# Optimization experiments

Hardware: AMD Instinct MI355X
Metric: run time of the kernel (lower is better)

Reference implementation:

```python
import jax, jax.numpy as jnp
import numpy as np

BATCH, BITS, HID = 65536, 64, 512
EPS = 1e-5

# M[s, i, j] = 1 if j == i - s  (left-shift-by-s permutation, causal)
_SHIFT_M = jnp.asarray(
    (np.arange(BITS)[None, :, None] - np.arange(BITS)[:, None, None]
     == np.arange(BITS)[None, None, :]).astype(np.float32))


def _layernorm(x, g, b):
    m = jnp.mean(x, axis=-1, keepdims=True)
    v = jnp.var(x, axis=-1, keepdims=True)
    return (x - m) * jax.lax.rsqrt(v + EPS) * g + b


def setup_inputs() -> dict:
    key = jax.random.key(0)
    ks = jax.random.split(key, 8)
    inp = {
        'a_bits': jax.random.uniform(ks[0], (BATCH, BITS), dtype=jnp.float32),
        'shift_bits': jax.random.uniform(ks[1], (BATCH, BITS), dtype=jnp.float32),
        # shift_decoder params: Linear(64,512) -> LN -> GELU -> Linear(512,512) -> LN -> GELU -> Linear(512,64)
        'W1': jax.random.normal(ks[2], (BITS, HID), dtype=jnp.float32) * (1.0 / np.sqrt(BITS)),
        'b1': jnp.zeros((HID,), jnp.float32),
        'g1': jnp.ones((HID,), jnp.float32),
        'be1': jnp.zeros((HID,), jnp.float32),
        'W2': jax.random.normal(ks[3], (HID, HID), dtype=jnp.float32) * (1.0 / np.sqrt(HID)),
        'b2': jnp.zeros((HID,), jnp.float32),
        'g2': jnp.ones((HID,), jnp.float32),
        'be2': jnp.zeros((HID,), jnp.float32),
        'W3': jax.random.normal(ks[4], (HID, BITS), dtype=jnp.float32) * (1.0 / np.sqrt(HID)),
        'b3': jnp.zeros((BITS,), jnp.float32),
    }
    return inp


def reference(a_bits, shift_bits, W1, b1, g1, be1, W2, b2, g2, be2, W3, b3):
    temperature = jnp.float32(1.0)
    # shift decoder MLP
    h = jax.nn.gelu(_layernorm(shift_bits @ W1 + b1, g1, be1), approximate=False)
    h = jax.nn.gelu(_layernorm(h @ W2 + b2, g2, be2), approximate=False)
    shift_logits = (h @ W3 + b3)[:, :BITS]
    # training path: soft shift distribution
    shift_probs = jax.nn.softmax(shift_logits / temperature, axis=-1)
    # weighted permutation matrix, then batched matvec (faithful to einsum+bmm)
    M_weighted = jnp.einsum('bs,sij->bij', shift_probs, _SHIFT_M)
    output = jnp.einsum('bij,bj->bi', M_weighted, a_bits)
    return output
```

## Files before the change

kernel.cpp:

```cpp
#include <hip/hip_runtime.h>
#include <hip/hip_bf16.h>
#include <math.h>

#define BATCH 65536
#define NT 512
#define BM 32

using f32x4 = __attribute__((ext_vector_type(4))) float;
using s16x8 = __attribute__((ext_vector_type(8))) short;

#define MFMA16(a, b, c) __builtin_amdgcn_mfma_f32_16x16x32_bf16((a), (b), (c), 0, 0, 0)

__device__ __forceinline__ unsigned short f2bf(float f) {
    unsigned u = __builtin_bit_cast(unsigned, f);
    u = u + 0x7FFFu + ((u >> 16) & 1u);
    return (unsigned short)(u >> 16);
}
__device__ __forceinline__ float bf2f(unsigned short h) {
    unsigned u = ((unsigned)h) << 16;
    return __builtin_bit_cast(float, u);
}

__device__ __forceinline__ float fast_erf(float x) {
    float ax = fabsf(x);
    float t = __builtin_amdgcn_rcpf(fmaf(0.3275911f, ax, 1.0f));
    float poly = t * fmaf(t, fmaf(t, fmaf(t, fmaf(t, 1.061405429f, -1.453152027f),
                                          1.421413741f), -0.284496736f), 0.254829592f);
    float r = 1.0f - poly * __expf(-ax * ax);
    return copysignf(r, x);
}
__device__ __forceinline__ float gelu(float y) {
    return 0.5f * y * (1.0f + fast_erf(y * 0.70710678118654752f));
}

__device__ __forceinline__ int hswz(int row, int k) {
    return row * 1024 + ((((k >> 3) ^ (row & 7))) << 4) + ((k & 7) << 1);
}
__device__ __forceinline__ int xaddr(int base, int row, int k) {
    return base + row * 128 + ((((k >> 3) ^ (row & 7))) << 4) + ((k & 7) << 1);
}

__global__ void weights_frag(const float* __restrict__ W1, const float* __restrict__ W2,
                             const float* __restrict__ W3, unsigned short* __restrict__ wt) {
    int b = blockIdx.x;
    int lane = threadIdx.x;
    const float* src; unsigned short* dst; int N, fragidx;
    if (b < 64)       { src = W1; dst = wt;          N = 512; fragidx = b; }
    else if (b < 576) { src = W2; dst = wt + 32768;  N = 512; fragidx = b - 64; }
    else              { src = W3; dst = wt + 294912; N = 64;  fragidx = b - 576; }
    int nt, ks;
    if (b < 64) { nt = fragidx >> 1; ks = fragidx & 1; }
    else        { nt = fragidx >> 4; ks = fragidx & 15; }
    int n  = nt * 16 + (lane & 15);
    int k0 = ks * 32 + (lane >> 4) * 8;
    unsigned short o[8];
#pragma unroll
    for (int e = 0; e < 8; e++) o[e] = f2bf(src[(size_t)(k0 + e) * N + n]);
    *(uint4*)(dst + ((size_t)fragidx * 64 + lane) * 8) = *(uint4*)o;
}

__device__ __forceinline__ void ln_partials(f32x4 (&acc)[2][4], char* smem, int redb,
                                            int ln, int g, int wave) {
#pragma unroll
    for (int fm = 0; fm < 2; fm++)
#pragma unroll
        for (int r = 0; r < 4; r++) {
            float s = 0.f, q = 0.f;
#pragma unroll
            for (int fn = 0; fn < 4; fn++) { float v = acc[fm][fn][r]; s += v; q += v * v; }
#pragma unroll
            for (int m = 1; m < 16; m <<= 1) { s += __shfl_xor(s, m, 64); q += __shfl_xor(q, m, 64); }
            if (ln == 0) {
                int row = fm * 16 + g * 4 + r;
                float* rp = (float*)(smem + redb + (row * 8 + wave) * 8);
                rp[0] = s; rp[1] = q;
            }
        }
}

#define SMEM_K1 39168
__global__ __launch_bounds__(NT, 6) void k1_gemm1(
    const float* __restrict__ shift_bits,
    const float* __restrict__ b1, const float* __restrict__ g1, const float* __restrict__ be1,
    const unsigned short* __restrict__ wt, unsigned short* __restrict__ h1,
    int rowoff) {
    __shared__ char smem[SMEM_K1];
    const int t = threadIdx.x;
    const int wave = t >> 6, lane = t & 63, g = lane >> 4, ln = lane & 15;
    const int row0 = rowoff + blockIdx.x * BM;
    const int lrow0 = blockIdx.x * BM;
    const int n0w = wave * 64;
    const int XB = 32768, RB = 36864, SB = 38912;
    const unsigned short* wt1f = wt;

    {
        int r = t >> 4, c = t & 15;
        float4 x = *(const float4*)(shift_bits + (size_t)(row0 + r) * 64 + c * 4);
        unsigned p0 = (unsigned)f2bf(x.x) | ((unsigned)f2bf(x.y) << 16);
        unsigned p1 = (unsigned)f2bf(x.z) | ((unsigned)f2bf(x.w) << 16);
        uint2 v; v.x = p0; v.y = p1;
        *(uint2*)(smem + XB + r * 128 + (((c >> 1) ^ (r & 7)) << 4) + (c & 1) * 8) = v;
    }
    __syncthreads();

    f32x4 acc[2][4];
#pragma unroll
    for (int fm = 0; fm < 2; fm++)
#pragma unroll
        for (int fn = 0; fn < 4; fn++) acc[fm][fn] = (f32x4){0.f, 0.f, 0.f, 0.f};
#pragma unroll
    for (int ks = 0; ks < 2; ks++) {
        s16x8 af[2], bf[4];
#pragma unroll
        for (int fn = 0; fn < 4; fn++) {
            int fragidx = (wave * 4 + fn) * 2 + ks;
            bf[fn] = *(const s16x8*)(wt1f + ((size_t)fragidx * 64 + lane) * 8);
        }
#pragma unroll
        for (int fm = 0; fm < 2; fm++)
            af[fm] = *(const s16x8*)(smem + xaddr(XB, fm * 16 + ln, ks * 32 + g * 8));
#pragma unroll
        for (int fm = 0; fm < 2; fm++)
#pragma unroll
            for (int fn = 0; fn < 4; fn++) acc[fm][fn] = MFMA16(af[fm], bf[fn], acc[fm][fn]);
    }

    {
        float bb[4];
#pragma unroll
        for (int fn = 0; fn < 4; fn++) bb[fn] = b1[n0w + fn * 16 + ln];
#pragma unroll
        for (int fm = 0; fm < 2; fm++)
#pragma unroll
            for (int fn = 0; fn < 4; fn++)
#pragma unroll
                for (int r = 0; r < 4; r++) acc[fm][fn][r] += bb[fn];
    }
    ln_partials(acc, smem, RB, ln, g, wave);
    __syncthreads();
    if (t < 32) {
        float s = 0.f, q = 0.f;
#pragma unroll
        for (int w = 0; w < 8; w++) {
            float* rp = (float*)(smem + RB + (t * 8 + w) * 8);
            s += rp[0]; q += rp[1];
        }
        float mu = s * (1.0f / 512.0f);
        float var = q * (1.0f / 512.0f) - mu * mu;
        float rs = rsqrtf(var + 1e-5f);
        float* sp = (float*)(smem + SB + t * 8);
        sp[0] = mu; sp[1] = rs;
    }
    __syncthreads();
    {
        float gm[4], bt[4];
#pragma unroll
        for (int fn = 0; fn < 4; fn++) { int c = n0w + fn * 16 + ln; gm[fn] = g1[c]; bt[fn] = be1[c]; }
#pragma unroll
        for (int fm = 0; fm < 2; fm++)
#pragma unroll
            for (int r = 0; r < 4; r++) {
                int row = fm * 16 + g * 4 + r;
                float* sp = (float*)(smem + SB + row * 8);
                float mu = sp[0], rs = sp[1];
#pragma unroll
                for (int fn = 0; fn < 4; fn++) {
                    int col = n0w + fn * 16 + ln;
                    float y = (acc[fm][fn][r] - mu) * rs * gm[fn] + bt[fn];
                    *(unsigned short*)(smem + hswz(row, col)) = f2bf(gelu(y));
                }
            }
    }
    __syncthreads();
    {
        int r = t >> 4, c0 = (t & 15) * 32;
        unsigned short* dst = h1 + (size_t)(lrow0 + r) * 512 + c0;
#pragma unroll
        for (int j = 0; j < 4; j++) {
            int gr = (c0 >> 3) + j;
            uint4 v = *(const uint4*)(smem + r * 1024 + ((gr ^ (r & 7)) << 4));
            *(uint4*)(dst + j * 8) = v;
        }
    }
}

#define SMEM_K2 35072
__global__ __launch_bounds__(NT, 4) void k2_gemm2(
    const unsigned short* __restrict__ h1, const float* __restrict__ b2,
    const float* __restrict__ g2, const float* __restrict__ be2,
    const unsigned short* __restrict__ wt, unsigned short* __restrict__ h2) {
    __shared__ char smem[SMEM_K2];
    const int t = threadIdx.x;
    const int wave = t >> 6, lane = t & 63, g = lane >> 4, ln = lane & 15;
    const int lrow0 = blockIdx.x * BM;
    const int n0w = wave * 64;
    const int RB = 32768, SB = 34816;
    const unsigned short* wt2f = wt + 32768;

    {
        int r = t >> 4, c0 = (t & 15) * 32;
        const unsigned short* src = h1 + (size_t)(lrow0 + r) * 512 + c0;
#pragma unroll
        for (int j = 0; j < 4; j++) {
            uint4 v = *(const uint4*)(src + j * 8);
            int gr = (c0 >> 3) + j;
            *(uint4*)(smem + r * 1024 + ((gr ^ (r & 7)) << 4)) = v;
        }
    }

    const unsigned short* bp[4];
#pragma unroll
    for (int fn = 0; fn < 4; fn++)
        bp[fn] = wt2f + ((size_t)(wave * 4 + fn) * 16 * 64 + lane) * 8;

    __syncthreads();

    f32x4 acc[2][4];
#pragma unroll
    for (int fm = 0; fm < 2; fm++)
#pragma unroll
        for (int fn = 0; fn < 4; fn++) acc[fm][fn] = (f32x4){0.f, 0.f, 0.f, 0.f};
    {
        s16x8 bpipe[3][4];
#pragma unroll
        for (int d = 0; d < 2; d++)
#pragma unroll
            for (int fn = 0; fn < 4; fn++)
                bpipe[d][fn] = *(const s16x8*)(bp[fn] + (size_t)d * 512);
#pragma unroll
        for (int step = 0; step < 16; step++) {
            if (step + 2 < 16) {
#pragma unroll
                for (int fn = 0; fn < 4; fn++)
                    bpipe[(step + 2) % 3][fn] = *(const s16x8*)(bp[fn] + (size_t)(step + 2) * 512);
            }
            s16x8 af[2];
#pragma unroll
            for (int fm = 0; fm < 2; fm++)
                af[fm] = *(const s16x8*)(smem + hswz(fm * 16 + ln, step * 32 + g * 8));
#pragma unroll
            for (int fm = 0; fm < 2; fm++)
#pragma unroll
                for (int fn = 0; fn < 4; fn++)
                    acc[fm][fn] = MFMA16(af[fm], bpipe[step % 3][fn], acc[fm][fn]);
        }
    }

    {
        float bb[4];
#pragma unroll
        for (int fn = 0; fn < 4; fn++) bb[fn] = b2[n0w + fn * 16 + ln];
#pragma unroll
        for (int fm = 0; fm < 2; fm++)
#pragma unroll
            for (int fn = 0; fn < 4; fn++)
#pragma unroll
                for (int r = 0; r < 4; r++) acc[fm][fn][r] += bb[fn];
    }
    ln_partials(acc, smem, RB, ln, g, wave);
    __syncthreads();
    if (t < 32) {
        float s = 0.f, q = 0.f;
#pragma unroll
        for (int w = 0; w < 8; w++) {
            float* rp = (float*)(smem + RB + (t * 8 + w) * 8);
            s += rp[0]; q += rp[1];
        }
        float mu = s * (1.0f / 512.0f);
        float var = q * (1.0f / 512.0f) - mu * mu;
        float rs = rsqrtf(var + 1e-5f);
        float* sp = (float*)(smem + SB + t * 8);
        sp[0] = mu; sp[1] = rs;
    }
    __syncthreads();

    {
        float gm[4], bt[4];
#pragma unroll
        for (int fn = 0; fn < 4; fn++) { int c = n0w + fn * 16 + ln; gm[fn] = g2[c]; bt[fn] = be2[c]; }
#pragma unroll
        for (int fm = 0; fm < 2; fm++)
#pragma unroll
            for (int r = 0; r < 4; r++) {
                int row = fm * 16 + g * 4 + r;
                float* sp = (float*)(smem + SB + row * 8);
                float mu = sp[0], rs = sp[1];
#pragma unroll
                for (int fn = 0; fn < 4; fn++) {
                    int col = n0w + fn * 16 + ln;
                    float y = (acc[fm][fn][r] - mu) * rs * gm[fn] + bt[fn];
                    *(unsigned short*)(smem + hswz(row, col)) = f2bf(gelu(y));
                }
            }
    }
    __syncthreads();
    {
        int r = t >> 4, c0 = (t & 15) * 32;
        unsigned short* dst = h2 + (size_t)(lrow0 + r) * 512 + c0;
#pragma unroll
        for (int j = 0; j < 4; j++) {
            int gr = (c0 >> 3) + j;
            uint4 v = *(const uint4*)(smem + r * 1024 + ((gr ^ (r & 7)) << 4));
            *(uint4*)(dst + j * 8) = v;
        }
    }
}

#define SMEM_K3 32768
__global__ __launch_bounds__(NT, 6) void k3_head(
    const unsigned short* __restrict__ h2, const float* __restrict__ a_bits,
    const float* __restrict__ b3, const unsigned short* __restrict__ wt,
    float* __restrict__ out, int rowoff) {
    __shared__ char smem[SMEM_K3];
    const int t = threadIdx.x;
    const int wave = t >> 6, lane = t & 63, g = lane >> 4, ln = lane & 15;
    const int lrow0 = blockIdx.x * BM;
    const int row0 = rowoff + lrow0;
    const unsigned short* wt3f = wt + 294912;

    {
        int r = t >> 4, c0 = (t & 15) * 32;
        const unsigned short* src = h2 + (size_t)(lrow0 + r) * 512 + c0;
#pragma unroll
        for (int j = 0; j < 4; j++) {
            uint4 v = *(const uint4*)(src + j * 8);
            int gr = (c0 >> 3) + j;
            *(uint4*)(smem + r * 1024 + ((gr ^ (r & 7)) << 4)) = v;
        }
    }
    __syncthreads();

    const int mh = wave >> 2, q = wave & 3;
    float b3v = b3[q * 16 + ln];
    const unsigned short* b3p = wt3f + ((size_t)q * 16 * 64 + lane) * 8;
    f32x4 acc3a = (f32x4){0.f, 0.f, 0.f, 0.f};
    f32x4 acc3b = (f32x4){0.f, 0.f, 0.f, 0.f};
#pragma unroll
    for (int ks = 0; ks < 16; ks += 2) {
        s16x8 bfr0 = *(const s16x8*)(b3p + (size_t)ks * 512);
        s16x8 bfr1 = *(const s16x8*)(b3p + (size_t)(ks + 1) * 512);
        s16x8 af0 = *(const s16x8*)(smem + hswz(mh * 16 + ln, ks * 32 + g * 8));
        s16x8 af1 = *(const s16x8*)(smem + hswz(mh * 16 + ln, (ks + 1) * 32 + g * 8));
        acc3a = MFMA16(af0, bfr0, acc3a);
        acc3b = MFMA16(af1, bfr1, acc3b);
    }
    __syncthreads();

    const int LOGB = 0, ABUF = 8704, LST = 272, AST = 544;
#pragma unroll
    for (int r = 0; r < 4; r++) {
        int row = mh * 16 + g * 4 + r;
        *(float*)(smem + LOGB + row * LST + (q * 16 + ln) * 4) = acc3a[r] + acc3b[r] + b3v;
    }
    {
        int r = t >> 4, c0 = (t & 15) * 4;
        float* ap = (float*)(smem + ABUF + r * AST);
        float4 z4 = {0.f, 0.f, 0.f, 0.f};
        *(float4*)(ap + c0) = z4;
        float4 av = *(const float4*)(a_bits + (size_t)(row0 + r) * 64 + c0);
        *(float4*)(ap + 64 + c0) = av;
    }
    __syncthreads();

    {
        int r = t >> 4, c0 = (t & 15) * 4;
        float* lp = (float*)(smem + LOGB + r * LST + c0 * 4);
        float4 v = *(float4*)lp;
        float mx = fmaxf(fmaxf(v.x, v.y), fmaxf(v.z, v.w));
#pragma unroll
        for (int d = 1; d < 16; d <<= 1) mx = fmaxf(mx, __shfl_xor(mx, d, 64));
        float e0 = __expf(v.x - mx), e1 = __expf(v.y - mx);
        float e2 = __expf(v.z - mx), e3 = __expf(v.w - mx);
        float s = e0 + e1 + e2 + e3;
#pragma unroll
        for (int d = 1; d < 16; d <<= 1) s += __shfl_xor(s, d, 64);
        float inv = 1.0f / s;
        float4 o; o.x = e0 * inv; o.y = e1 * inv; o.z = e2 * inv; o.w = e3 * inv;
        *(float4*)lp = o;
    }
    __syncthreads();

    {
        int r = t >> 4, i0 = (t & 15) * 4;
        const float* prow = (const float*)(smem + LOGB + r * LST);
        const float* apad = (const float*)(smem + ABUF + r * AST);
        float W[8];
        {
            float4 wa = *(const float4*)(apad + i0 + 60);
            float4 wb = *(const float4*)(apad + i0 + 64);
            W[0] = wa.x; W[1] = wa.y; W[2] = wa.z; W[3] = wa.w;
            W[4] = wb.x; W[5] = wb.y; W[6] = wb.z; W[7] = wb.w;
        }
        float o0 = 0.f, o1 = 0.f, o2 = 0.f, o3 = 0.f;
#pragma unroll
        for (int s4 = 0; s4 < 16; s4++) {
            float4 p4 = *(const float4*)(prow + 4 * s4);
            o0 = fmaf(p4.x, W[4], fmaf(p4.y, W[3], fmaf(p4.z, W[2], fmaf(p4.w, W[1], o0))));
            o1 = fmaf(p4.x, W[5], fmaf(p4.y, W[4], fmaf(p4.z, W[3], fmaf(p4.w, W[2], o1))));
            o2 = fmaf(p4.x, W[6], fmaf(p4.y, W[5], fmaf(p4.z, W[4], fmaf(p4.w, W[3], o2))));
            o3 = fmaf(p4.x, W[7], fmaf(p4.y, W[6], fmaf(p4.z, W[5], fmaf(p4.w, W[4], o3))));
            if (s4 < 15) {
                W[4] = W[0]; W[5] = W[1]; W[6] = W[2]; W[7] = W[3];
                float4 nw = *(const float4*)(apad + i0 + 56 - 4 * s4);
                W[0] = nw.x; W[1] = nw.y; W[2] = nw.z; W[3] = nw.w;
            }
        }
        float4 o; o.x = o0; o.y = o1; o.z = o2; o.w = o3;
        *(float4*)(out + (size_t)(row0 + r) * 64 + i0) = o;
    }
}

extern "C" void kernel_launch(void* const* d_in, const int* in_sizes, int n_in,
                              void* d_out, int out_size, void* d_ws, size_t ws_size,
                              hipStream_t stream) {
    const float* a_bits = (const float*)d_in[0];
    const float* shift  = (const float*)d_in[1];
    const float* W1  = (const float*)d_in[2];
    const float* b1  = (const float*)d_in[3];
    const float* g1  = (const float*)d_in[4];
    const float* be1 = (const float*)d_in[5];
    const float* W2  = (const float*)d_in[6];
    const float* b2  = (const float*)d_in[7];
    const float* g2  = (const float*)d_in[8];
    const float* be2 = (const float*)d_in[9];
    const float* W3  = (const float*)d_in[10];
    const float* b3  = (const float*)d_in[11];
    float* out = (float*)d_out;

    char* ws = (char*)d_ws;
    unsigned short* wt = (unsigned short*)ws;

    int CH = 1;
    while (CH < 32) {
        size_t need = 655360ull + 2048ull * (size_t)(BATCH / CH);
        if (need <= ws_size) break;
        CH *= 2;
    }
    const int chunk = BATCH / CH;
    unsigned short* h1 = (unsigned short*)(ws + 655360);
    unsigned short* h2 = h1 + (size_t)chunk * 512;

    weights_frag<<<640, 64, 0, stream>>>(W1, W2, W3, wt);
    for (int c = 0; c < CH; c++) {
        int rowoff = c * chunk;
        k1_gemm1<<<chunk / BM, NT, 0, stream>>>(shift, b1, g1, be1, wt, h1, rowoff);
        k2_gemm2<<<chunk / BM, NT, 0, stream>>>(h1, b2, g2, be2, wt, h2);
        k3_head<<<chunk / BM, NT, 0, stream>>>(h2, a_bits, b3, wt, out, rowoff);
    }
}
```

Before: 172.2 us.

## Fuse second GEMM and head kernels, keeping h2 in shared memory

Merges the layer-2 GEMM+LN+GELU kernel with the head GEMM+softmax+shift kernel so the bf16 h2 activations stay in LDS instead of being written to and re-read from global memory. This removes one kernel launch per chunk and roughly 64 MB of global traffic, and halves the workspace need, which may allow larger chunks. The weight prefetch is also changed from a 3-deep to a 2-deep register pipeline, which lowers register pressure but hides less load latency. The fused kernel runs at the lower occupancy bound of the GEMM2 kernel, whereas the head kernel previously allowed more blocks per CU.

```diff
diff --git a/kernel.cpp b/kernel.cpp
--- a/kernel.cpp
+++ b/kernel.cpp
@@ -15,10 +15,6 @@
     unsigned u = __builtin_bit_cast(unsigned, f);
     u = u + 0x7FFFu + ((u >> 16) & 1u);
     return (unsigned short)(u >> 16);
-}
-__device__ __forceinline__ float bf2f(unsigned short h) {
-    unsigned u = ((unsigned)h) << 16;
-    return __builtin_bit_cast(float, u);
 }
 
 __device__ __forceinline__ float fast_erf(float x) {
@@ -184,18 +180,20 @@
     }
 }
 
-#define SMEM_K2 35072
-__global__ __launch_bounds__(NT, 4) void k2_gemm2(
-    const unsigned short* __restrict__ h1, const float* __restrict__ b2,
-    const float* __restrict__ g2, const float* __restrict__ be2,
-    const unsigned short* __restrict__ wt, unsigned short* __restrict__ h2) {
-    __shared__ char smem[SMEM_K2];
+#define SMEM_K23 35072
+__global__ __launch_bounds__(NT, 4) void k23_fused(
+    const unsigned short* __restrict__ h1, const float* __restrict__ a_bits,
+    const float* __restrict__ b2, const float* __restrict__ g2, const float* __restrict__ be2,
+    const float* __restrict__ b3, const unsigned short* __restrict__ wt,
+    float* __restrict__ out, int rowoff) {
+    __shared__ char smem[SMEM_K23];
     const int t = threadIdx.x;
     const int wave = t >> 6, lane = t & 63, g = lane >> 4, ln = lane & 15;
     const int lrow0 = blockIdx.x * BM;
-    const int n0w = wave * 64;
+    const int row0 = rowoff + lrow0;
     const int RB = 32768, SB = 34816;
     const unsigned short* wt2f = wt + 32768;
+    const unsigned short* wt3f = wt + 294912;
 
     {
         int r = t >> 4, c0 = (t & 15) * 32;
@@ -208,6 +206,7 @@
         }
     }
 
+    const int n0w = wave * 64;
     const unsigned short* bp[4];
 #pragma unroll
     for (int fn = 0; fn < 4; fn++)
@@ -221,18 +220,15 @@
 #pragma unroll
         for (int fn = 0; fn < 4; fn++) acc[fm][fn] = (f32x4){0.f, 0.f, 0.f, 0.f};
     {
-        s16x8 bpipe[3][4];
-#pragma unroll
-        for (int d = 0; d < 2; d++)
-#pragma unroll
-            for (int fn = 0; fn < 4; fn++)
-                bpipe[d][fn] = *(const s16x8*)(bp[fn] + (size_t)d * 512);
+        s16x8 bcur[4], bnxt[4];
+#pragma unroll
+        for (int fn = 0; fn < 4; fn++) bcur[fn] = *(const s16x8*)(bp[fn]);
 #pragma unroll
         for (int step = 0; step < 16; step++) {
-            if (step + 2 < 16) {
+            if (step < 15) {
 #pragma unroll
                 for (int fn = 0; fn < 4; fn++)
-                    bpipe[(step + 2) % 3][fn] = *(const s16x8*)(bp[fn] + (size_t)(step + 2) * 512);
+                    bnxt[fn] = *(const s16x8*)(bp[fn] + (size_t)(step + 1) * 512);
             }
             s16x8 af[2];
 #pragma unroll
@@ -241,8 +237,9 @@
 #pragma unroll
             for (int fm = 0; fm < 2; fm++)
 #pragma unroll
-                for (int fn = 0; fn < 4; fn++)
-                    acc[fm][fn] = MFMA16(af[fm], bpipe[step % 3][fn], acc[fm][fn]);
+                for (int fn = 0; fn < 4; fn++) acc[fm][fn] = MFMA16(af[fm], bcur[fn], acc[fm][fn]);
+#pragma unroll
+            for (int fn = 0; fn < 4; fn++) bcur[fn] = bnxt[fn];
         }
     }
 
@@ -292,41 +289,6 @@
                     *(unsigned short*)(smem + hswz(row, col)) = f2bf(gelu(y));
                 }
             }
-    }
-    __syncthreads();
-    {
-        int r = t >> 4, c0 = (t & 15) * 32;
-        unsigned short* dst = h2 + (size_t)(lrow0 + r) * 512 + c0;
-#pragma unroll
-        for (int j = 0; j < 4; j++) {
-            int gr = (c0 >> 3) + j;
-            uint4 v = *(const uint4*)(smem + r * 1024 + ((gr ^ (r & 7)) << 4));
-            *(uint4*)(dst + j * 8) = v;
-        }
-    }
-}
-
-#define SMEM_K3 32768
-__global__ __launch_bounds__(NT, 6) void k3_head(
-    const unsigned short* __restrict__ h2, const float* __restrict__ a_bits,
-    const float* __restrict__ b3, const unsigned short* __restrict__ wt,
-    float* __restrict__ out, int rowoff) {
-    __shared__ char smem[SMEM_K3];
-    const int t = threadIdx.x;
-    const int wave = t >> 6, lane = t & 63, g = lane >> 4, ln = lane & 15;
-    const int lrow0 = blockIdx.x * BM;
-    const int row0 = rowoff + lrow0;
-    const unsigned short* wt3f = wt + 294912;
-
-    {
-        int r = t >> 4, c0 = (t & 15) * 32;
-        const unsigned short* src = h2 + (size_t)(lrow0 + r) * 512 + c0;
-#pragma unroll
-        for (int j = 0; j < 4; j++) {
-            uint4 v = *(const uint4*)(src + j * 8);
-            int gr = (c0 >> 3) + j;
-            *(uint4*)(smem + r * 1024 + ((gr ^ (r & 7)) << 4)) = v;
-        }
     }
     __syncthreads();
 
@@ -432,19 +394,17 @@
 
     int CH = 1;
     while (CH < 32) {
-        size_t need = 655360ull + 2048ull * (size_t)(BATCH / CH);
+        size_t need = 655360ull + 1024ull * (size_t)(BATCH / CH);
         if (need <= ws_size) break;
         CH *= 2;
     }
     const int chunk = BATCH / CH;
     unsigned short* h1 = (unsigned short*)(ws + 655360);
-    unsigned short* h2 = h1 + (size_t)chunk * 512;
 
     weights_frag<<<640, 64, 0, stream>>>(W1, W2, W3, wt);
     for (int c = 0; c < CH; c++) {
         int rowoff = c * chunk;
         k1_gemm1<<<chunk / BM, NT, 0, stream>>>(shift, b1, g1, be1, wt, h1, rowoff);
-        k2_gemm2<<<chunk / BM, NT, 0, stream>>>(h1, b2, g2, be2, wt, h2);
-        k3_head<<<chunk / BM, NT, 0, stream>>>(h2, a_bits, b3, wt, out, rowoff);
-    }
-}
+        k23_fused<<<chunk / BM, NT, 0, stream>>>(h1, a_bits, b2, g2, be2, b3, wt, out, rowoff);
+    }
+}
```

Result: faster. 144.3 us (-16.2%).
